# Optimization experiments

Measured on AMD Instinct MI355X. Metric: run time of the kernel, lower is better.

Reference implementation:

```python
import jax, jax.numpy as jnp
import numpy as np

B, H, W, CH, CW, MAXINS = 8, 320, 1024, 3, 3, 200


def setup_inputs() -> dict:
    key = jax.random.key(0)
    k1, k2 = jax.random.split(key)
    # per-pixel instance id in [0, MAXINS)
    instance = jax.random.randint(k1, (B, 1, H, W), 0, MAXINS, dtype=jnp.int32)
    # per-pixel 3x3 matrices to be scatter-summed per instance
    compsrc = jax.random.normal(k2, (B, H, W, CH, CW), dtype=jnp.float32)
    return {"instance": instance, "compsrc": compsrc, "maxinsnum": MAXINS}


def reference(instance, compsrc, maxinsnum):
    """EPPCore compress-then-inflate.

    epp_compression: compdst[b, ins] = sum over pixels {(h,w): instance[b,0,h,w]==ins} of 1.1*compsrc[b,h,w]
    epp_inflation:   infdst[b,h,w]  = compdst[b, instance[b,0,h,w]]
    """
    bz, h, w, ch, cw = compsrc.shape
    idx = instance[:, 0].reshape(bz, h * w)                 # [B, HW] int32 segment ids
    src = (compsrc * 1.1).reshape(bz, h * w, ch * cw)       # note: original forward scales by 1.1
    # per-batch scatter-sum over instance ids -> [B, maxinsnum, ch*cw]
    comp = jax.vmap(
        lambda i, s: jax.ops.segment_sum(s, i, num_segments=maxinsnum)
    )(idx, src)
    comp = comp.reshape(bz, maxinsnum, ch, cw)              # [B, maxinsnum, 3, 3]
    # inflation: per-pixel gather of the per-instance matrix -> [B, H, W, 3, 3]
    inf = jax.vmap(lambda c, i: c[i])(comp, instance[:, 0])
    return inf
```

## Files before the change

### kernel.cpp

```cpp
#include <hip/hip_runtime.h>

#define BATCH   8
#define HW      (320 * 1024)
#define ELEMS   (HW * 9)
#define MAXINS  200
#define BINS    (MAXINS * 9)
#define NXBLK   256
#define SCALE      2097152.0f
#define INV_SCALE_D (1.1 / 2097152.0)

__device__ __forceinline__ void decode8(int e, int& pix0, int& pix1,
                                        int& j0, int& b) {
    pix0 = e / 9;
    j0   = e - pix0 * 9;
    b    = 9 - j0;
    pix1 = (e + 7) / 9;
}

__global__ __launch_bounds__(256) void epp_compress(
    const int* __restrict__ inst, const float* __restrict__ src,
    int* __restrict__ compi)
{
    __shared__ int bins[BINS];
    const int b = blockIdx.y;

    for (int i = threadIdx.x; i < BINS; i += 256) bins[i] = 0;
    __syncthreads();

    const int total8 = ELEMS / 8;
    const int* __restrict__ instb = inst + b * HW;
    const float4* __restrict__ srcb = (const float4*)(src + (size_t)b * ELEMS);
    const int stride = NXBLK * 256;

    for (int g = blockIdx.x * 256 + threadIdx.x; g < total8; g += stride) {
        float4 v0 = srcb[2 * g];
        float4 v1 = srcb[2 * g + 1];
        const int e = g * 8;
        int pix0, pix1, j0, cnt;
        decode8(e, pix0, pix1, j0, cnt);
        const int id0 = instb[pix0] * 9 + j0;
        const int id1 = instb[pix1] * 9 + j0 - 9;
        float vals[8] = {v0.x, v0.y, v0.z, v0.w, v1.x, v1.y, v1.z, v1.w};
#pragma unroll
        for (int k = 0; k < 8; ++k) {
            int base = (k < cnt) ? id0 : id1;
            int q = __float2int_rn(vals[k] * SCALE);
            atomicAdd(&bins[base + k], q);
        }
    }
    __syncthreads();

    int* __restrict__ cb = compi + b * BINS;
    for (int i = threadIdx.x; i < BINS; i += 256) {
        atomicAdd(&cb[i], bins[i]);
    }
}

__global__ __launch_bounds__(256) void epp_inflate(
    const int* __restrict__ inst, const int* __restrict__ compi,
    float* __restrict__ out)
{
    __shared__ float bins[BINS];
    const int b = blockIdx.y;
    const int* __restrict__ cb = compi + b * BINS;
    for (int i = threadIdx.x; i < BINS; i += 256) {
        bins[i] = (float)((double)cb[i] * INV_SCALE_D);
    }
    __syncthreads();

    const int total8 = ELEMS / 8;
    const int* __restrict__ instb = inst + b * HW;
    float4* __restrict__ outb = (float4*)(out + (size_t)b * ELEMS);
    const int stride = gridDim.x * 256;

    for (int g = blockIdx.x * 256 + threadIdx.x; g < total8; g += stride) {
        const int e = g * 8;
        int pix0, pix1, j0, cnt;
        decode8(e, pix0, pix1, j0, cnt);
        const int id0 = instb[pix0] * 9 + j0;
        const int id1 = instb[pix1] * 9 + j0 - 9;
        float vals[8];
#pragma unroll
        for (int k = 0; k < 8; ++k) {
            int base = (k < cnt) ? id0 : id1;
            vals[k] = bins[base + k];
        }
        outb[2 * g]     = make_float4(vals[0], vals[1], vals[2], vals[3]);
        outb[2 * g + 1] = make_float4(vals[4], vals[5], vals[6], vals[7]);
    }
}

extern "C" void kernel_launch(void* const* d_in, const int* in_sizes, int n_in,
                              void* d_out, int out_size, void* d_ws, size_t ws_size,
                              hipStream_t stream) {
    const int*   inst = (const int*)d_in[0];
    const float* src  = (const float*)d_in[1];
    float* out = (float*)d_out;

    const size_t compBytes = (size_t)BATCH * BINS * sizeof(int);
    if (ws_size < compBytes) return;

    int* compi = (int*)d_ws;

    (void)hipMemsetAsync(compi, 0, compBytes, stream);

    dim3 cgrid(NXBLK, BATCH);
    epp_compress<<<cgrid, 256, 0, stream>>>(inst, src, compi);

    dim3 igrid(512, BATCH);
    epp_inflate<<<igrid, 256, 0, stream>>>(inst, compi, out);
}
```

Measured before the change: 56.09 us.

## Process four pixels per thread in compress with padded 12-wide LDS bins

The compress kernel now gives each thread four whole pixels: it loads 9 float4 of source data and one int4 of instance ids, so all bin indices are known at compile time and the per-element divide and select go away. LDS bins are padded to 12 entries per instance to change the bank mapping, and each block handles a fixed chunk of 512 quads with 160 blocks per batch instead of a grid-stride loop. This relies on 160*512*4 exactly covering HW, and it reduces parallelism per batch while raising per-thread register pressure.

```diff
diff --git a/kernel.cpp b/kernel.cpp
--- a/kernel.cpp
+++ b/kernel.cpp
@@ -5,7 +5,9 @@
 #define ELEMS   (HW * 9)
 #define MAXINS  200
 #define BINS    (MAXINS * 9)
-#define NXBLK   256
+#define LBINS   (MAXINS * 12)
+#define NXBLK   160
+#define QPB     512
 #define SCALE      2097152.0f
 #define INV_SCALE_D (1.1 / 2097152.0)
 
@@ -21,38 +23,47 @@
     const int* __restrict__ inst, const float* __restrict__ src,
     int* __restrict__ compi)
 {
-    __shared__ int bins[BINS];
+    __shared__ int bins[LBINS];
     const int b = blockIdx.y;
 
-    for (int i = threadIdx.x; i < BINS; i += 256) bins[i] = 0;
+    for (int i = threadIdx.x; i < LBINS; i += 256) bins[i] = 0;
     __syncthreads();
 
-    const int total8 = ELEMS / 8;
     const int* __restrict__ instb = inst + b * HW;
     const float4* __restrict__ srcb = (const float4*)(src + (size_t)b * ELEMS);
-    const int stride = NXBLK * 256;
+    const int q0 = blockIdx.x * QPB;
 
-    for (int g = blockIdx.x * 256 + threadIdx.x; g < total8; g += stride) {
-        float4 v0 = srcb[2 * g];
-        float4 v1 = srcb[2 * g + 1];
-        const int e = g * 8;
-        int pix0, pix1, j0, cnt;
-        decode8(e, pix0, pix1, j0, cnt);
-        const int id0 = instb[pix0] * 9 + j0;
-        const int id1 = instb[pix1] * 9 + j0 - 9;
-        float vals[8] = {v0.x, v0.y, v0.z, v0.w, v1.x, v1.y, v1.z, v1.w};
 #pragma unroll
-        for (int k = 0; k < 8; ++k) {
-            int base = (k < cnt) ? id0 : id1;
-            int q = __float2int_rn(vals[k] * SCALE);
-            atomicAdd(&bins[base + k], q);
+    for (int it = 0; it < 2; ++it) {
+        const int q = q0 + it * 256 + threadIdx.x;
+        const int p = q * 4;
+        const int4 ids = *(const int4*)(instb + p);
+        int base[4] = {ids.x * 12, ids.y * 12, ids.z * 12, ids.w * 12};
+
+        const float4* s = srcb + (size_t)q * 9;
+        float4 f[9];
+#pragma unroll
+        for (int r = 0; r < 9; ++r) f[r] = s[r];
+
+#pragma unroll
+        for (int r = 0; r < 9; ++r) {
+            const float v[4] = {f[r].x, f[r].y, f[r].z, f[r].w};
+#pragma unroll
+            for (int c = 0; c < 4; ++c) {
+                const int i  = 4 * r + c;
+                const int px = i / 9;
+                const int j  = i - px * 9;
+                atomicAdd(&bins[base[px] + j],
+                          __float2int_rn(v[c] * SCALE));
+            }
         }
     }
     __syncthreads();
 
     int* __restrict__ cb = compi + b * BINS;
     for (int i = threadIdx.x; i < BINS; i += 256) {
-        atomicAdd(&cb[i], bins[i]);
+        const int id = i / 9, j = i - id * 9;
+        atomicAdd(&cb[i], bins[id * 12 + j]);
     }
 }
 
@@ -75,14 +86,14 @@
 
     for (int g = blockIdx.x * 256 + threadIdx.x; g < total8; g += stride) {
         const int e = g * 8;
-        int pix0, pix1, j0, cnt;
-        decode8(e, pix0, pix1, j0, cnt);
+        int pix0, pix1, j0, cnt8;
+        decode8(e, pix0, pix1, j0, cnt8);
         const int id0 = instb[pix0] * 9 + j0;
         const int id1 = instb[pix1] * 9 + j0 - 9;
         float vals[8];
 #pragma unroll
         for (int k = 0; k < 8; ++k) {
-            int base = (k < cnt) ? id0 : id1;
+            int base = (k < cnt8) ? id0 : id1;
             vals[k] = bins[base + k];
         }
         outb[2 * g]     = make_float4(vals[0], vals[1], vals[2], vals[3]);
```

Result: faster. 52.81 us (-5.8%).
